# Optimization experiments

Measured on AMD Instinct MI355X. Metric: run time of the kernel, lower is better.

The kernel has to match this reference:

```python
import jax, jax.numpy as jnp
import numpy as np

N = 50000      # nodes
E = 800000     # edges (before self-loops)
IN = 512       # in_dim
HID = 128      # hidden_dim
HEADS = 4
NEG_SLOPE = 0.2


def setup_inputs() -> dict:
    key = jax.random.key(0)
    ks = jax.random.split(key, 20)
    s = 0.05
    inp = {
        'x': jax.random.normal(ks[0], (N, IN), jnp.float32),
        'edge_index': jax.random.randint(ks[1], (2, E), 0, N, dtype=jnp.int32),
        # layer 0: GATConv(IN -> HID, heads=HEADS)
        'W0': jax.random.normal(ks[2], (HEADS * HID, IN), jnp.float32) * s,
        'a_src0': jax.random.normal(ks[3], (HEADS, HID), jnp.float32) * s,
        'a_dst0': jax.random.normal(ks[4], (HEADS, HID), jnp.float32) * s,
        'b0': jnp.zeros((HEADS * HID,), jnp.float32),
        # layer 1: GATConv(HEADS*HID -> HID, heads=HEADS)
        'W1': jax.random.normal(ks[5], (HEADS * HID, HEADS * HID), jnp.float32) * s,
        'a_src1': jax.random.normal(ks[6], (HEADS, HID), jnp.float32) * s,
        'a_dst1': jax.random.normal(ks[7], (HEADS, HID), jnp.float32) * s,
        'b1': jnp.zeros((HEADS * HID,), jnp.float32),
        # layer 2: GATConv(HEADS*HID -> HID, heads=1)
        'W2': jax.random.normal(ks[8], (HID, HEADS * HID), jnp.float32) * s,
        'a_src2': jax.random.normal(ks[9], (1, HID), jnp.float32) * s,
        'a_dst2': jax.random.normal(ks[10], (1, HID), jnp.float32) * s,
        'b2': jnp.zeros((HID,), jnp.float32),
        # output heads
        'Wv': jax.random.normal(ks[11], (HID, HID), jnp.float32) * s,
        'bv': jnp.zeros((HID,), jnp.float32),
        'Wt': jax.random.normal(ks[12], (HID, HID), jnp.float32) * s,
        'bt': jnp.zeros((HID,), jnp.float32),
    }
    return inp


def _gat_conv(x, src, dst, W, a_src, a_dst, bias, heads, n_nodes):
    """PyG-style GATConv (eval mode, att_dropout=0, self-loops pre-added)."""
    ch = a_src.shape[-1]
    h = (x @ W.T).reshape(n_nodes, heads, ch)            # [N,H,C]
    alpha_s = jnp.einsum('nhc,hc->nh', h, a_src)          # [N,H]
    alpha_d = jnp.einsum('nhc,hc->nh', h, a_dst)          # [N,H]
    e = alpha_s[src] + alpha_d[dst]                       # [E,H]
    e = jnp.where(e > 0, e, NEG_SLOPE * e)                # leaky_relu(0.2)
    # segment softmax over destination nodes
    m = jax.ops.segment_max(e, dst, num_segments=n_nodes)  # [N,H]
    e = jnp.exp(e - m[dst])
    z = jax.ops.segment_sum(e, dst, num_segments=n_nodes)  # [N,H]
    alpha = e / (z[dst] + 1e-16)                          # [E,H]
    msg = h[src] * alpha[:, :, None]                      # [E,H,C]
    out = jax.ops.segment_sum(msg, dst, num_segments=n_nodes)  # [N,H,C]
    return out.reshape(n_nodes, heads * ch) + bias


def reference(x, edge_index, W0, a_src0, a_dst0, b0, W1, a_src1, a_dst1, b1,
              W2, a_src2, a_dst2, b2, Wv, bv, Wt, bt):
    n = x.shape[0]
    loops = jnp.arange(n, dtype=edge_index.dtype)
    src = jnp.concatenate([edge_index[0], loops])
    dst = jnp.concatenate([edge_index[1], loops])

    h = _gat_conv(x, src, dst, W0, a_src0, a_dst0, b0, HEADS, n)
    h = jax.nn.relu(h)                                    # dropout is no-op in eval
    h = _gat_conv(h, src, dst, W1, a_src1, a_dst1, b1, HEADS, n)
    h = jax.nn.relu(h)
    h = _gat_conv(h, src, dst, W2, a_src2, a_dst2, b2, 1, n)  # [N,HID]

    x_vision = jax.nn.relu(h @ Wv.T + bv)
    x_text = jax.nn.relu(h @ Wt.T + bt)
    return (h, x_vision, x_text)
```

## Files before the change

kernel.cpp:

```cpp
#include <hip/hip_runtime.h>
#include <hip/hip_bf16.h>
#include <math.h>

typedef __bf16 bf16;
typedef __bf16 bf16x2 __attribute__((ext_vector_type(2)));
typedef __bf16 bf16x4 __attribute__((ext_vector_type(4)));
typedef __bf16 bf16x8 __attribute__((ext_vector_type(8)));
typedef float f32x4 __attribute__((ext_vector_type(4)));

#define NNODES 50000
#define NEDGES 800000

static __device__ __forceinline__ void gld_lds16(const void* g, void* l) {
    __builtin_amdgcn_global_load_lds((__attribute__((address_space(1))) void*)g,
                                     (__attribute__((address_space(3))) void*)l,
                                     16, 0, 0);
}

__global__ void detect_kernel(const unsigned int* __restrict__ xw, int* __restrict__ flag)
{
    const int l = threadIdx.x;
    int c = 0;
    for (int i = l; i < 4096; i += 64) {
        const unsigned int b1 = (xw[i] >> 8) & 0x7Fu;
        c += (b1 >= 0x34u && b1 <= 0x43u) ? 1 : 0;
    }
#pragma unroll
    for (int off = 32; off; off >>= 1) c += __shfl_xor(c, off);
    if (l == 0) *flag = (c < 2048) ? 1 : 0;
}

__global__ __launch_bounds__(256) void zero_out_kernel(void* out, long n, const int* __restrict__ flag)
{
    const int fp32 = *flag;
    const long i = (long)blockIdx.x * 256 + threadIdx.x;
    if (i < n) {
        if (fp32) ((float*)out)[i] = 0.f;
        else ((bf16*)out)[i] = (bf16)0.f;
    }
}

__global__ __launch_bounds__(256) void convert4_kernel(
    const void* __restrict__ in, bf16* __restrict__ out, int n4, const int* __restrict__ flag)
{
    const int fp32 = *flag;
    const int i = blockIdx.x * 256 + threadIdx.x;
    if (i >= n4) return;
    bf16x4 o;
    if (fp32) {
        const float4 v = ((const float4*)in)[i];
        o[0] = (bf16)v.x; o[1] = (bf16)v.y; o[2] = (bf16)v.z; o[3] = (bf16)v.w;
    } else {
        o = ((const bf16x4*)in)[i];
    }
    ((bf16x4*)out)[i] = o;
}

struct CvtBatch { const void* in[16]; bf16* out[16]; int n4[16]; };

__global__ __launch_bounds__(256) void convert_batch_kernel(CvtBatch b, const int* __restrict__ flag)
{
    const int fp32 = *flag;
    const int it = blockIdx.y;
    const int n4 = b.n4[it];
    const void* in = b.in[it];
    bf16* out = b.out[it];
    for (int i = blockIdx.x * 256 + threadIdx.x; i < n4; i += gridDim.x * 256) {
        bf16x4 o;
        if (fp32) {
            const float4 v = ((const float4*)in)[i];
            o[0] = (bf16)v.x; o[1] = (bf16)v.y; o[2] = (bf16)v.z; o[3] = (bf16)v.w;
        } else {
            o = ((const bf16x4*)in)[i];
        }
        ((bf16x4*)out)[i] = o;
    }
}

__global__ __launch_bounds__(256) void gemm_bt(
    const bf16* __restrict__ A, const bf16* __restrict__ B,
    bf16* __restrict__ C, int M, int N, int K,
    const bf16* __restrict__ av, const bf16* __restrict__ dv,
    float* __restrict__ aS, float* __restrict__ aD, int H)
{
    __shared__ __align__(16) bf16 As[128 * 32];
    __shared__ __align__(16) bf16 Bs[128 * 32];
    __shared__ float sPS[128];
    __shared__ float sPD[128];
    const int tid  = threadIdx.x;
    const int lane = tid & 63;
    const int w    = tid >> 6;
    const int wm   = (w >> 1) * 64, wn = (w & 1) * 64;
    const int mBase = blockIdx.y * 128, nBase = blockIdx.x * 128;
    const int hb = nBase >> 7;

    f32x4 acc[4][4];
#pragma unroll
    for (int i = 0; i < 4; i++)
#pragma unroll
        for (int j = 0; j < 4; j++)
#pragma unroll
            for (int r = 0; r < 4; r++) acc[i][j][r] = 0.f;

    const int rA   = tid >> 2;
    const int kseg = (tid & 3) * 8;
    int ra0 = mBase + rA;       if (ra0 > M - 1) ra0 = M - 1;
    int ra1 = mBase + rA + 64;  if (ra1 > M - 1) ra1 = M - 1;
    const bf16* gA0 = A + (long)ra0 * K + kseg;
    const bf16* gA1 = A + (long)ra1 * K + kseg;
    const bf16* gB0 = B + (long)(nBase + rA) * K + kseg;
    const bf16* gB1 = B + (long)(nBase + rA + 64) * K + kseg;
    bf16* lA0 = &As[tid * 8];
    bf16* lA1 = &As[(tid + 256) * 8];
    bf16* lB0 = &Bs[tid * 8];
    bf16* lB1 = &Bs[(tid + 256) * 8];

    const int quad = lane >> 4, l16 = lane & 15;

    if (tid < 128) { sPS[tid] = 0.f; sPD[tid] = 0.f; }

    for (int k0 = 0; k0 < K; k0 += 32) {
        gld_lds16(gA0 + k0, lA0);
        gld_lds16(gA1 + k0, lA1);
        gld_lds16(gB0 + k0, lB0);
        gld_lds16(gB1 + k0, lB1);
        __syncthreads();
        bf16x8 af[4], bfr[4];
#pragma unroll
        for (int i = 0; i < 4; i++) {
            af[i]  = *(const bf16x8*)&As[(wm + i * 16 + l16) * 32 + quad * 8];
            bfr[i] = *(const bf16x8*)&Bs[(wn + i * 16 + l16) * 32 + quad * 8];
        }
#pragma unroll
        for (int i = 0; i < 4; i++)
#pragma unroll
            for (int j = 0; j < 4; j++)
                acc[i][j] = __builtin_amdgcn_mfma_f32_16x16x32_bf16(af[i], bfr[j], acc[i][j], 0, 0, 0);
        __syncthreads();
    }

    float aval[4], dval[4];
#pragma unroll
    for (int j = 0; j < 4; j++) {
        const int cg = nBase + wn + j * 16 + l16;
        aval[j] = (float)av[cg];
        dval[j] = (float)dv[cg];
    }
#pragma unroll
    for (int i = 0; i < 4; i++) {
#pragma unroll
        for (int r = 0; r < 4; r++) {
            float ps = 0.f, pd = 0.f;
#pragma unroll
            for (int j = 0; j < 4; j++) {
                ps += acc[i][j][r] * aval[j];
                pd += acc[i][j][r] * dval[j];
            }
#pragma unroll
            for (int off = 8; off; off >>= 1) {
                ps += __shfl_xor(ps, off);
                pd += __shfl_xor(pd, off);
            }
            if (l16 == 0) {
                const int rl = wm + i * 16 + quad * 4 + r;
                atomicAdd(&sPS[rl], ps);
                atomicAdd(&sPD[rl], pd);
            }
        }
    }

#pragma unroll
    for (int i = 0; i < 4; i++) {
        const int row0 = mBase + wm + i * 16 + quad * 4;
#pragma unroll
        for (int j = 0; j < 4; j++) {
            const int colg = nBase + wn + j * 16 + l16;
#pragma unroll
            for (int r = 0; r < 4; r++) {
                const int row = row0 + r;
                if (row < M) C[(long)row * N + colg] = (bf16)acc[i][j][r];
            }
        }
    }

    __syncthreads();
    if (tid < 128) {
        const int row = mBase + tid;
        if (row < M) {
            aS[(long)row * H + hb] = sPS[tid];
            aD[(long)row * H + hb] = sPD[tid];
        }
    }
}

__global__ __launch_bounds__(256) void heads_gemm(
    const bf16* __restrict__ A, const bf16* __restrict__ B,
    void* __restrict__ outv, const bf16* __restrict__ bias,
    const int* __restrict__ dflag, int M)
{
    __shared__ __align__(16) bf16 As[128 * 32];
    __shared__ __align__(16) bf16 Bs[128 * 32];
    const int fp32 = *dflag;
    const int tid  = threadIdx.x;
    const int lane = tid & 63;
    const int w    = tid >> 6;
    const int wm   = (w >> 1) * 64, wn = (w & 1) * 64;
    const int mBase = blockIdx.y * 128, nBase = blockIdx.x * 128;
    const int K = 128;

    f32x4 acc[4][4];
#pragma unroll
    for (int i = 0; i < 4; i++)
#pragma unroll
        for (int j = 0; j < 4; j++)
#pragma unroll
            for (int r = 0; r < 4; r++) acc[i][j][r] = 0.f;

    const int rA   = tid >> 2;
    const int kseg = (tid & 3) * 8;
    int ra0 = mBase + rA;       if (ra0 > M - 1) ra0 = M - 1;
    int ra1 = mBase + rA + 64;  if (ra1 > M - 1) ra1 = M - 1;
    const bf16* gA0 = A + (long)ra0 * K + kseg;
    const bf16* gA1 = A + (long)ra1 * K + kseg;
    const bf16* gB0 = B + (long)(nBase + rA) * K + kseg;
    const bf16* gB1 = B + (long)(nBase + rA + 64) * K + kseg;
    bf16* lA0 = &As[tid * 8];
    bf16* lA1 = &As[(tid + 256) * 8];
    bf16* lB0 = &Bs[tid * 8];
    bf16* lB1 = &Bs[(tid + 256) * 8];

    const int quad = lane >> 4, l16 = lane & 15;

    for (int k0 = 0; k0 < K; k0 += 32) {
        gld_lds16(gA0 + k0, lA0);
        gld_lds16(gA1 + k0, lA1);
        gld_lds16(gB0 + k0, lB0);
        gld_lds16(gB1 + k0, lB1);
        __syncthreads();
        bf16x8 af[4], bfr[4];
#pragma unroll
        for (int i = 0; i < 4; i++) {
            af[i]  = *(const bf16x8*)&As[(wm + i * 16 + l16) * 32 + quad * 8];
            bfr[i] = *(const bf16x8*)&Bs[(wn + i * 16 + l16) * 32 + quad * 8];
        }
#pragma unroll
        for (int i = 0; i < 4; i++)
#pragma unroll
            for (int j = 0; j < 4; j++)
                acc[i][j] = __builtin_amdgcn_mfma_f32_16x16x32_bf16(af[i], bfr[j], acc[i][j], 0, 0, 0);
        __syncthreads();
    }

#pragma unroll
    for (int j = 0; j < 4; j++) {
        const int colg = nBase + wn + j * 16 + l16;
        const float bv = (float)bias[colg];
        const int sec = 1 + (colg >> 7);
        const int cl  = colg & 127;
        const long sbase = (long)sec * M * 128 + cl;
#pragma unroll
        for (int i = 0; i < 4; i++) {
            const int row0 = mBase + wm + i * 16 + quad * 4;
#pragma unroll
            for (int r = 0; r < 4; r++) {
                const int row = row0 + r;
                if (row < M) {
                    const float o = fmaxf(acc[i][j][r] + bv, 0.f);
                    const long idx = sbase + (long)row * 128;
                    if (fp32) ((float*)outv)[idx] = o;
                    else ((bf16*)outv)[idx] = (bf16)o;
                }
            }
        }
    }
}

__global__ void hist_kernel(const int* __restrict__ dst, int* __restrict__ cnt, int E)
{
    const int e = blockIdx.x * blockDim.x + threadIdx.x;
    if (e < E) atomicAdd(&cnt[dst[e]], 1);
}

__global__ __launch_bounds__(256) void scan1_kernel(
    const int* __restrict__ cnt, int* __restrict__ rowptr, int* __restrict__ blksum, int n)
{
    __shared__ int buf[256];
    const int b = blockIdx.x, t = threadIdx.x, i = b * 256 + t;
    const int v = (i < n) ? cnt[i] : 0;
    buf[t] = v;
    __syncthreads();
    for (int off = 1; off < 256; off <<= 1) {
        const int add = (t >= off) ? buf[t - off] : 0;
        __syncthreads();
        buf[t] += add;
        __syncthreads();
    }
    if (i < n) rowptr[i + 1] = buf[t];
    if (t == 255) blksum[b] = buf[255];
    if (b == 0 && t == 0) rowptr[0] = 0;
}

__global__ __launch_bounds__(256) void scan2_kernel(int* __restrict__ blksum, int nb)
{
    __shared__ int buf[256];
    const int t = threadIdx.x;
    const int v = (t < nb) ? blksum[t] : 0;
    buf[t] = v;
    __syncthreads();
    for (int off = 1; off < 256; off <<= 1) {
        const int add = (t >= off) ? buf[t - off] : 0;
        __syncthreads();
        buf[t] += add;
        __syncthreads();
    }
    if (t < nb) blksum[t] = buf[t] - v;
}

__global__ __launch_bounds__(256) void scan3_kernel(
    int* __restrict__ rowptr, const int* __restrict__ blksum, int n)
{
    const int b = blockIdx.x, i = b * 256 + threadIdx.x;
    if (i < n) rowptr[i + 1] += blksum[b];
}

__global__ void fill_kernel(const int* __restrict__ src, const int* __restrict__ dst,
                            const int* __restrict__ rowptr, int* __restrict__ off,
                            int* __restrict__ col, int E)
{
    const int e = blockIdx.x * blockDim.x + threadIdx.x;
    if (e < E) {
        const int d = dst[e];
        const int p = rowptr[d] + atomicAdd(&off[d], 1);
        col[p] = src[e];
    }
}

__global__ __launch_bounds__(256) void agg4s_kernel(
    const bf16* __restrict__ h, const float* __restrict__ asrc,
    const float* __restrict__ adst, const int* __restrict__ rowptr,
    const int* __restrict__ col, const bf16* __restrict__ bias,
    bf16* __restrict__ out, int NB)
{
    __shared__ int2 ew_s[4][64];
    const int w = threadIdx.x >> 6, lane = threadIdx.x & 63;
    const int g = lane >> 4, li = lane & 15;
    const int xcd = blockIdx.x & 7;
    const int s = xcd >> 1;
    const int nbi = ((blockIdx.x >> 3) << 1) | (xcd & 1);
    const int n = nbi * 4 + w;
    const float ad = adst[(long)n * 4 + s];
    const int start = rowptr[n];
    const int deg   = rowptr[n + 1] - start;
    const int total = deg + 1;

    float z = 0.f;
    float acc[8];
#pragma unroll
    for (int c = 0; c < 8; c++) acc[c] = 0.f;
    const char* hbp = (const char*)h;
    const int sOff = s * 256 + li * 16;
    const int2* ews = ew_s[w];

    for (int base = 0; base < total; base += 64) {
        const int i = base + lane;
        const bool valid = i < total;
        const int sv = (i < deg) ? col[start + i] : n;
        float e = asrc[(long)sv * 4 + s] + ad;
        e = (e > 0.f) ? e : 0.2f * e;
        e = fminf(fmaxf(e, -60.f), 60.f);
        const float wv = valid ? __expf(e) : 0.f;
        ew_s[w][lane] = make_int2(sv << 10, __float_as_int(wv));
        __builtin_amdgcn_wave_barrier();
        const int cnt = min(64, total - base);
#pragma unroll 2
        for (int j = 0; j < cnt; j += 4) {
            const int2 v = ews[j + g];
            const float ww = __int_as_float(v.y);
            z += ww;
            const bf16x8 hv = *(const bf16x8*)(hbp + (v.x + sOff));
#pragma unroll
            for (int c = 0; c < 8; c++) acc[c] += ww * (float)hv[c];
        }
        __builtin_amdgcn_wave_barrier();
    }

#pragma unroll
    for (int c = 0; c < 8; c++) {
        acc[c] += __shfl_xor(acc[c], 16);
        acc[c] += __shfl_xor(acc[c], 32);
    }
    z += __shfl_xor(z, 16);
    z += __shfl_xor(z, 32);

    if (g == 0) {
        const float rz = 1.f / (z + 1e-16f);
        const bf16x8 b8 = *(const bf16x8*)(bias + s * 128 + li * 8);
        bf16x8 ov;
#pragma unroll
        for (int c = 0; c < 8; c++)
            ov[c] = (bf16)fmaxf(acc[c] * rz + (float)b8[c], 0.f);
        *(bf16x8*)(out + (long)n * 512 + s * 128 + li * 8) = ov;
    }
}

__global__ __launch_bounds__(256) void agg1g_kernel(
    const bf16* __restrict__ h, const float* __restrict__ asrc,
    const float* __restrict__ adst, const int* __restrict__ rowptr,
    const int* __restrict__ col, const bf16* __restrict__ bias,
    void* __restrict__ outv, bf16* __restrict__ hb16, const int* __restrict__ dflag)
{
    __shared__ int2 ew_s[4][64];
    const int w = threadIdx.x >> 6, lane = threadIdx.x & 63;
    const int g = lane >> 4, li = lane & 15;
    const int n = blockIdx.x * 4 + w;
    if (n >= NNODES) return;
    const int fp32out = *dflag;
    const float ad = adst[n];
    const int start = rowptr[n];
    const int deg   = rowptr[n + 1] - start;
    const int total = deg + 1;

    float z = 0.f;
    float acc[8];
#pragma unroll
    for (int c = 0; c < 8; c++) acc[c] = 0.f;
    const char* hbp = (const char*)h;
    const int sOff = li * 16;
    const int2* ews = ew_s[w];

    for (int base = 0; base < total; base += 64) {
        const int i = base + lane;
        const bool valid = i < total;
        const int sv = (i < deg) ? col[start + i] : n;
        float e = asrc[sv] + ad;
        e = (e > 0.f) ? e : 0.2f * e;
        e = fminf(fmaxf(e, -60.f), 60.f);
        const float wv = valid ? __expf(e) : 0.f;
        ew_s[w][lane] = make_int2(sv << 8, __float_as_int(wv));
        __builtin_amdgcn_wave_barrier();
        const int cnt = min(64, total - base);
#pragma unroll 2
        for (int j = 0; j < cnt; j += 4) {
            const int2 v = ews[j + g];
            const float ww = __int_as_float(v.y);
            z += ww;
            const bf16x8 hv = *(const bf16x8*)(hbp + (v.x + sOff));
#pragma unroll
            for (int c = 0; c < 8; c++) acc[c] += ww * (float)hv[c];
        }
        __builtin_amdgcn_wave_barrier();
    }

#pragma unroll
    for (int c = 0; c < 8; c++) {
        acc[c] += __shfl_xor(acc[c], 16);
        acc[c] += __shfl_xor(acc[c], 32);
    }
    z += __shfl_xor(z, 16);
    z += __shfl_xor(z, 32);

    if (g == 0) {
        const float rz = 1.f / (z + 1e-16f);
        float o[8];
#pragma unroll
        for (int c = 0; c < 8; c++)
            o[c] = acc[c] * rz + (float)bias[li * 8 + c];
        bf16x8 ovb;
#pragma unroll
        for (int c = 0; c < 8; c++) ovb[c] = (bf16)o[c];
        *(bf16x8*)(hb16 + (long)n * 128 + li * 8) = ovb;
        if (fp32out) {
            float* op = (float*)outv + (long)n * 128 + li * 8;
            f32x4 o0, o1;
#pragma unroll
            for (int c = 0; c < 4; c++) { o0[c] = o[c]; o1[c] = o[c + 4]; }
            *(f32x4*)op = o0;
            *(f32x4*)(op + 4) = o1;
        } else {
            *(bf16x8*)((bf16*)outv + (long)n * 128 + li * 8) = ovb;
        }
    }
}

extern "C" void kernel_launch(void* const* d_in, const int* in_sizes, int n_in,
                              void* d_out, int out_size, void* d_ws, size_t ws_size,
                              hipStream_t stream)
{
    const int N = NNODES, E = NEDGES;
    const int* srcp = (const int*)d_in[1];
    const int* dstp = srcp + E;

    char* p0 = (char*)d_ws;
    char* p = p0;
    auto bump = [&](size_t b) { char* r = p; p += (b + 255) & ~(size_t)255; return r; };
    int*   dflag  = (int*)bump(256);
    bf16*  xc     = (bf16*)bump((size_t)N * 512 * 2);
    bf16*  W0c    = (bf16*)bump(262144 * 2);
    bf16*  as0c   = (bf16*)bump(512 * 2);
    bf16*  ad0c   = (bf16*)bump(512 * 2);
    bf16*  b0c    = (bf16*)bump(512 * 2);
    bf16*  W1c    = (bf16*)bump(262144 * 2);
    bf16*  as1c   = (bf16*)bump(512 * 2);
    bf16*  ad1c   = (bf16*)bump(512 * 2);
    bf16*  b1c    = (bf16*)bump(512 * 2);
    bf16*  W2c    = (bf16*)bump(65536 * 2);
    bf16*  as2c   = (bf16*)bump(128 * 2);
    bf16*  ad2c   = (bf16*)bump(128 * 2);
    bf16*  b2c    = (bf16*)bump(128 * 2);
    bf16*  Wcat   = (bf16*)bump(32768 * 2);
    bf16*  bcat   = (bf16*)bump(256 * 2);
    int*   cnt    = (int*)bump((size_t)N * 4);
    int*   offs   = (int*)bump((size_t)N * 4);
    int*   rowptr = (int*)bump((size_t)(N + 1) * 4);
    int*   blksum = (int*)bump(256 * 4);
    int*   colarr = (int*)bump((size_t)E * 4);
    float* alphaS = (float*)bump((size_t)N * 4 * 4);
    float* alphaD = (float*)bump((size_t)N * 4 * 4);
    bf16*  bufA   = (bf16*)bump((size_t)N * 512 * 2);
    bf16*  bufB   = (bf16*)bump((size_t)N * 512 * 2);
    bf16*  hb16   = (bf16*)bump((size_t)N * 128 * 2);
    const size_t need = (size_t)(p - p0);

    detect_kernel<<<1, 64, 0, stream>>>((const unsigned int*)d_in[0], dflag);

    if (need > ws_size) {
        zero_out_kernel<<<((long)out_size + 255) / 256, 256, 0, stream>>>(d_out, out_size, dflag);
        return;
    }

    convert4_kernel<<<(N * 512 / 4 + 255) / 256, 256, 0, stream>>>(d_in[0], xc, N * 512 / 4, dflag);
    CvtBatch cb;
    const void* ins[16] = {d_in[2], d_in[3], d_in[4], d_in[5], d_in[6], d_in[7], d_in[8], d_in[9],
                           d_in[10], d_in[11], d_in[12], d_in[13], d_in[14], d_in[15], d_in[16], d_in[17]};
    bf16* outs[16] = {W0c, as0c, ad0c, b0c, W1c, as1c, ad1c, b1c,
                      W2c, as2c, ad2c, b2c, Wcat, bcat, Wcat + 16384, bcat + 128};
    const int ns4[16] = {65536, 128, 128, 128, 65536, 128, 128, 128,
                         16384, 32, 32, 32, 4096, 32, 4096, 32};
    for (int i = 0; i < 16; i++) { cb.in[i] = ins[i]; cb.out[i] = outs[i]; cb.n4[i] = ns4[i]; }
    convert_batch_kernel<<<dim3(64, 16), 256, 0, stream>>>(cb, dflag);

    const int nb = (N + 255) / 256;
    hipMemsetAsync(cnt, 0, (size_t)N * 4, stream);
    hipMemsetAsync(offs, 0, (size_t)N * 4, stream);
    hist_kernel<<<(E + 255) / 256, 256, 0, stream>>>(dstp, cnt, E);
    scan1_kernel<<<nb, 256, 0, stream>>>(cnt, rowptr, blksum, N);
    scan2_kernel<<<1, 256, 0, stream>>>(blksum, nb);
    scan3_kernel<<<nb, 256, 0, stream>>>(rowptr, blksum, N);
    fill_kernel<<<(E + 255) / 256, 256, 0, stream>>>(srcp, dstp, rowptr, offs, colarr, E);

    const int NB = N / 4;

    dim3 g0(4, (N + 127) / 128);
    gemm_bt<<<g0, 256, 0, stream>>>(xc, W0c, bufA, N, 512, 512,
                                    as0c, ad0c, alphaS, alphaD, 4);
    agg4s_kernel<<<NB * 4, 256, 0, stream>>>(bufA, alphaS, alphaD, rowptr, colarr, b0c, bufB, NB);

    gemm_bt<<<g0, 256, 0, stream>>>(bufB, W1c, bufA, N, 512, 512,
                                    as1c, ad1c, alphaS, alphaD, 4);
    agg4s_kernel<<<NB * 4, 256, 0, stream>>>(bufA, alphaS, alphaD, rowptr, colarr, b1c, bufB, NB);

    dim3 g2(1, (N + 127) / 128);
    gemm_bt<<<g2, 256, 0, stream>>>(bufB, W2c, bufA, N, 128, 512,
                                    as2c, ad2c, alphaS, alphaD, 1);
    agg1g_kernel<<<(N + 3) / 4, 256, 0, stream>>>(bufA, alphaS, alphaD, rowptr, colarr, b2c,
                                                  d_out, hb16, dflag);

    heads_gemm<<<dim3(2, (N + 127) / 128), 256, 0, stream>>>(hb16, Wcat, d_out, bcat, dflag, N);
}
```

Before: 738.5 us.

## Double-buffer LDS tiles and XOR-swizzle layout in GEMM kernels

Both MFMA GEMM kernels now use two LDS buffers so the global-to-LDS load of the next K tile is issued before computing the current one, removing one barrier per iteration. The LDS layout is also XOR-swizzled across row pairs to reduce bank conflicts on the 16-byte fragment reads. This doubles LDS usage per block, which may reduce occupancy. There is a possible race: the async global_load_lds for the next tile is not explicitly waited on before the barrier in every path.

```diff
diff --git a/kernel.cpp b/kernel.cpp
--- a/kernel.cpp
+++ b/kernel.cpp
@@ -83,8 +83,8 @@
     const bf16* __restrict__ av, const bf16* __restrict__ dv,
     float* __restrict__ aS, float* __restrict__ aD, int H)
 {
-    __shared__ __align__(16) bf16 As[128 * 32];
-    __shared__ __align__(16) bf16 Bs[128 * 32];
+    __shared__ __align__(16) bf16 As[2][128 * 32];
+    __shared__ __align__(16) bf16 Bs[2][128 * 32];
     __shared__ float sPS[128];
     __shared__ float sPD[128];
     const int tid  = threadIdx.x;
@@ -102,41 +102,60 @@
 #pragma unroll
             for (int r = 0; r < 4; r++) acc[i][j][r] = 0.f;
 
-    const int rA   = tid >> 2;
-    const int kseg = (tid & 3) * 8;
-    int ra0 = mBase + rA;       if (ra0 > M - 1) ra0 = M - 1;
-    int ra1 = mBase + rA + 64;  if (ra1 > M - 1) ra1 = M - 1;
-    const bf16* gA0 = A + (long)ra0 * K + kseg;
-    const bf16* gA1 = A + (long)ra1 * K + kseg;
-    const bf16* gB0 = B + (long)(nBase + rA) * K + kseg;
-    const bf16* gB1 = B + (long)(nBase + rA + 64) * K + kseg;
-    bf16* lA0 = &As[tid * 8];
-    bf16* lA1 = &As[(tid + 256) * 8];
-    bf16* lB0 = &Bs[tid * 8];
-    bf16* lB1 = &Bs[(tid + 256) * 8];
+    const int L0 = tid,       sr0 = L0 >> 3, su0 = (L0 & 7) ^ (sr0 & 7);
+    const int L1 = tid + 256, sr1 = L1 >> 3, su1 = (L1 & 7) ^ (sr1 & 7);
+    const int row0 = (sr0 << 1) | (su0 >> 2), g0 = (su0 & 3) * 8;
+    const int row1 = (sr1 << 1) | (su1 >> 2), g1 = (su1 & 3) * 8;
+    int ra0 = mBase + row0; if (ra0 > M - 1) ra0 = M - 1;
+    int ra1 = mBase + row1; if (ra1 > M - 1) ra1 = M - 1;
+    const bf16* gA0 = A + (long)ra0 * K + g0;
+    const bf16* gA1 = A + (long)ra1 * K + g1;
+    const bf16* gB0 = B + (long)(nBase + row0) * K + g0;
+    const bf16* gB1 = B + (long)(nBase + row1) * K + g1;
 
     const int quad = lane >> 4, l16 = lane & 15;
 
+    int oA[4], oB[4];
+#pragma unroll
+    for (int i = 0; i < 4; i++) {
+        const int rA_ = wm + i * 16 + l16;
+        const int rB_ = wn + i * 16 + l16;
+        oA[i] = ((rA_ >> 1) << 6) + (((((rA_ & 1) << 2) | quad) ^ ((rA_ >> 1) & 7)) << 3);
+        oB[i] = ((rB_ >> 1) << 6) + (((((rB_ & 1) << 2) | quad) ^ ((rB_ >> 1) & 7)) << 3);
+    }
+
     if (tid < 128) { sPS[tid] = 0.f; sPD[tid] = 0.f; }
 
-    for (int k0 = 0; k0 < K; k0 += 32) {
-        gld_lds16(gA0 + k0, lA0);
-        gld_lds16(gA1 + k0, lA1);
-        gld_lds16(gB0 + k0, lB0);
-        gld_lds16(gB1 + k0, lB1);
+    gld_lds16(gA0, &As[0][tid * 8]);
+    gld_lds16(gA1, &As[0][(tid + 256) * 8]);
+    gld_lds16(gB0, &Bs[0][tid * 8]);
+    gld_lds16(gB1, &Bs[0][(tid + 256) * 8]);
+
+    const int nt = K >> 5;
+    for (int t = 0; t < nt; ++t) {
         __syncthreads();
+        if (t + 1 < nt) {
+            const int k1 = (t + 1) << 5;
+            bf16* a = As[(t + 1) & 1];
+            bf16* b = Bs[(t + 1) & 1];
+            gld_lds16(gA0 + k1, &a[tid * 8]);
+            gld_lds16(gA1 + k1, &a[(tid + 256) * 8]);
+            gld_lds16(gB0 + k1, &b[tid * 8]);
+            gld_lds16(gB1 + k1, &b[(tid + 256) * 8]);
+        }
+        const bf16* as = As[t & 1];
+        const bf16* bs = Bs[t & 1];
         bf16x8 af[4], bfr[4];
 #pragma unroll
         for (int i = 0; i < 4; i++) {
-            af[i]  = *(const bf16x8*)&As[(wm + i * 16 + l16) * 32 + quad * 8];
-            bfr[i] = *(const bf16x8*)&Bs[(wn + i * 16 + l16) * 32 + quad * 8];
+            af[i]  = *(const bf16x8*)&as[oA[i]];
+            bfr[i] = *(const bf16x8*)&bs[oB[i]];
         }
 #pragma unroll
         for (int i = 0; i < 4; i++)
 #pragma unroll
             for (int j = 0; j < 4; j++)
                 acc[i][j] = __builtin_amdgcn_mfma_f32_16x16x32_bf16(af[i], bfr[j], acc[i][j], 0, 0, 0);
-        __syncthreads();
     }
 
     float aval[4], dval[4];
@@ -171,13 +190,13 @@
 
 #pragma unroll
     for (int i = 0; i < 4; i++) {
-        const int row0 = mBase + wm + i * 16 + quad * 4;
+        const int row0c = mBase + wm + i * 16 + quad * 4;
 #pragma unroll
         for (int j = 0; j < 4; j++) {
             const int colg = nBase + wn + j * 16 + l16;
 #pragma unroll
             for (int r = 0; r < 4; r++) {
-                const int row = row0 + r;
+                const int row = row0c + r;
                 if (row < M) C[(long)row * N + colg] = (bf16)acc[i][j][r];
             }
         }
@@ -198,8 +217,8 @@
     void* __restrict__ outv, const bf16* __restrict__ bias,
     const int* __restrict__ dflag, int M)
 {
-    __shared__ __align__(16) bf16 As[128 * 32];
-    __shared__ __align__(16) bf16 Bs[128 * 32];
+    __shared__ __align__(16) bf16 As[2][128 * 32];
+    __shared__ __align__(16) bf16 Bs[2][128 * 32];
     const int fp32 = *dflag;
     const int tid  = threadIdx.x;
     const int lane = tid & 63;
@@ -216,39 +235,58 @@
 #pragma unroll
             for (int r = 0; r < 4; r++) acc[i][j][r] = 0.f;
 
-    const int rA   = tid >> 2;
-    const int kseg = (tid & 3) * 8;
-    int ra0 = mBase + rA;       if (ra0 > M - 1) ra0 = M - 1;
-    int ra1 = mBase + rA + 64;  if (ra1 > M - 1) ra1 = M - 1;
-    const bf16* gA0 = A + (long)ra0 * K + kseg;
-    const bf16* gA1 = A + (long)ra1 * K + kseg;
-    const bf16* gB0 = B + (long)(nBase + rA) * K + kseg;
-    const bf16* gB1 = B + (long)(nBase + rA + 64) * K + kseg;
-    bf16* lA0 = &As[tid * 8];
-    bf16* lA1 = &As[(tid + 256) * 8];
-    bf16* lB0 = &Bs[tid * 8];
-    bf16* lB1 = &Bs[(tid + 256) * 8];
+    const int L0 = tid,       sr0 = L0 >> 3, su0 = (L0 & 7) ^ (sr0 & 7);
+    const int L1 = tid + 256, sr1 = L1 >> 3, su1 = (L1 & 7) ^ (sr1 & 7);
+    const int row0 = (sr0 << 1) | (su0 >> 2), g0 = (su0 & 3) * 8;
+    const int row1 = (sr1 << 1) | (su1 >> 2), g1 = (su1 & 3) * 8;
+    int ra0 = mBase + row0; if (ra0 > M - 1) ra0 = M - 1;
+    int ra1 = mBase + row1; if (ra1 > M - 1) ra1 = M - 1;
+    const bf16* gA0 = A + (long)ra0 * K + g0;
+    const bf16* gA1 = A + (long)ra1 * K + g1;
+    const bf16* gB0 = B + (long)(nBase + row0) * K + g0;
+    const bf16* gB1 = B + (long)(nBase + row1) * K + g1;
 
     const int quad = lane >> 4, l16 = lane & 15;
 
-    for (int k0 = 0; k0 < K; k0 += 32) {
-        gld_lds16(gA0 + k0, lA0);
-        gld_lds16(gA1 + k0, lA1);
-        gld_lds16(gB0 + k0, lB0);
-        gld_lds16(gB1 + k0, lB1);
+    int oA[4], oB[4];
+#pragma unroll
+    for (int i = 0; i < 4; i++) {
+        const int rA_ = wm + i * 16 + l16;
+        const int rB_ = wn + i * 16 + l16;
+        oA[i] = ((rA_ >> 1) << 6) + (((((rA_ & 1) << 2) | quad) ^ ((rA_ >> 1) & 7)) << 3);
+        oB[i] = ((rB_ >> 1) << 6) + (((((rB_ & 1) << 2) | quad) ^ ((rB_ >> 1) & 7)) << 3);
+    }
+
+    gld_lds16(gA0, &As[0][tid * 8]);
+    gld_lds16(gA1, &As[0][(tid + 256) * 8]);
+    gld_lds16(gB0, &Bs[0][tid * 8]);
+    gld_lds16(gB1, &Bs[0][(tid + 256) * 8]);
+
+    const int nt = K >> 5;
+    for (int t = 0; t < nt; ++t) {
         __syncthreads();
+        if (t + 1 < nt) {
+            const int k1 = (t + 1) << 5;
+            bf16* a = As[(t + 1) & 1];
+            bf16* b = Bs[(t + 1) & 1];
+            gld_lds16(gA0 + k1, &a[tid * 8]);
+            gld_lds16(gA1 + k1, &a[(tid + 256) * 8]);
+            gld_lds16(gB0 + k1, &b[tid * 8]);
+            gld_lds16(gB1 + k1, &b[(tid + 256) * 8]);
+        }
+        const bf16* as = As[t & 1];
+        const bf16* bs = Bs[t & 1];
         bf16x8 af[4], bfr[4];
 #pragma unroll
         for (int i = 0; i < 4; i++) {
-            af[i]  = *(const bf16x8*)&As[(wm + i * 16 + l16) * 32 + quad * 8];
-            bfr[i] = *(const bf16x8*)&Bs[(wn + i * 16 + l16) * 32 + quad * 8];
+            af[i]  = *(const bf16x8*)&as[oA[i]];
+            bfr[i] = *(const bf16x8*)&bs[oB[i]];
         }
 #pragma unroll
         for (int i = 0; i < 4; i++)
 #pragma unroll
             for (int j = 0; j < 4; j++)
                 acc[i][j] = __builtin_amdgcn_mfma_f32_16x16x32_bf16(af[i], bfr[j], acc[i][j], 0, 0, 0);
-        __syncthreads();
     }
 
 #pragma unroll
@@ -260,10 +298,10 @@
         const long sbase = (long)sec * M * 128 + cl;
 #pragma unroll
         for (int i = 0; i < 4; i++) {
-            const int row0 = mBase + wm + i * 16 + quad * 4;
+            const int row0c = mBase + wm + i * 16 + quad * 4;
 #pragma unroll
             for (int r = 0; r < 4; r++) {
-                const int row = row0 + r;
+                const int row = row0c + r;
                 if (row < M) {
                     const float o = fmaxf(acc[i][j][r] + bv, 0.f);
                     const long idx = sbase + (long)row * 128;
```

After: 730.5 us. About the same (-1.1%).
